# Optimization experiments

Measured on AMD Instinct MI355X. Metric: run time of the kernel, lower is better.

Reference implementation:

```python
import jax, jax.numpy as jnp
import numpy as np

B, T, N, C = 64, 256, 21, 3
HID, HEADS, HDIM, DOUT = 128, 4, 32, 256
CDIM, DMODEL = 64, 256
DINNER, DSTATE, DCONV, DTRANK, L = 512, 16, 4, 16, 4
NSIGNS, NHS, NLOC, NMOV, NORI = 2000, 40, 20, 20, 8
TEMP = 0.07

def _ln(x, w):
    mu = x.mean(-1, keepdims=True)
    var = ((x - mu) ** 2).mean(-1, keepdims=True)
    return (x - mu) / jnp.sqrt(var + 1e-5) * w

def _silu(x):
    return x * jax.nn.sigmoid(x)

def _causal_conv(u, w, b):  # u:(B,T,D), depthwise causal conv, w:(D,K)
    K = w.shape[1]
    up = jnp.pad(u, ((0, 0), (K - 1, 0), (0, 0)))
    y = sum(up[:, k:k + u.shape[1], :] * w[:, k] for k in range(K))
    return y + b

def _scan(u, dt, Bm, Cm, A, Dp):  # selective SSM scan; u,dt:(B,T,Di), Bm,Cm:(B,T,Ds)
    def step(h, xs):
        dt_t, b_t, c_t, u_t = xs
        dA = jnp.exp(dt_t[..., None] * A)                       # (B,Di,Ds)
        dBu = dt_t[..., None] * b_t[:, None, :] * u_t[..., None]
        h = dA * h + dBu
        y = jnp.einsum('bds,bs->bd', h, c_t)
        return h, y
    h0 = jnp.zeros((u.shape[0], A.shape[0], A.shape[1]), u.dtype)
    xs = (dt.swapaxes(0, 1), Bm.swapaxes(0, 1), Cm.swapaxes(0, 1), u.swapaxes(0, 1))
    _, ys = jax.lax.scan(step, h0, xs)
    return ys.swapaxes(0, 1) + u * Dp

def _cos_logits(f, p):
    fn = f / (jnp.linalg.norm(f, axis=-1, keepdims=True) + 1e-8)
    pn = p / (jnp.linalg.norm(p, axis=-1, keepdims=True) + 1e-8)
    return fn @ pn.T / TEMP

def _forward(x, agan_w_in, agan_b_in, agan_w_gat, agan_a_src, agan_a_dst,
             agan_w_out, agan_b_out, pdm_w, pdm_b, pdm_w_fuse, pdm_b_fuse,
             ssm_ln_w, ssm_in_proj, ssm_conv_w, ssm_conv_b, ssm_x_proj,
             ssm_dt_w, ssm_dt_b, ssm_A_log, ssm_D, ssm_out_proj,
             hpc_w_sign, hpc_b_sign, sign_protos, proto_hs, proto_loc,
             proto_mov, proto_ori):
    # ---- AGAN: multi-head graph attention over N landmarks per frame ----
    h0 = jax.nn.relu(x @ agan_w_in + agan_b_in)                  # (B,T,N,HID)
    h = jnp.einsum('btni,hio->btnho', h0, agan_w_gat)            # (B,T,N,H,O)
    src = jnp.einsum('btnho,ho->btnh', h, agan_a_src)
    dst = jnp.einsum('btnho,ho->btnh', h, agan_a_dst)
    e = jax.nn.leaky_relu(src[:, :, :, None, :] + dst[:, :, None, :, :], 0.2)  # (B,T,Ni,Nj,H)
    alpha = jax.nn.softmax(e, axis=3)
    agg = jnp.einsum('btijh,btjho->btiho', alpha, h).reshape(h0.shape)
    feat = jax.nn.relu(h0 + agg)
    spatial = (feat @ agan_w_out + agan_b_out).mean(axis=2)      # (B,T,DOUT)
    # ---- PDM: 4 phonological component projections + fusion ----
    comps = jax.nn.relu(jnp.einsum('btd,kdc->btkc', spatial, pdm_w) + pdm_b)  # (B,T,4,CDIM)
    fused = comps.reshape(B, T, 4 * CDIM) @ pdm_w_fuse + pdm_b_fuse           # (B,T,DMODEL)
    # ---- BiSSM: bidirectional selective SSM layers with residuals ----
    xx = fused
    for l in range(L):
        xn = _ln(xx, ssm_ln_w[l])
        ysum = 0.0
        for d in range(2):
            u_in = xn if d == 0 else xn[:, ::-1]
            xz = u_in @ ssm_in_proj[l, d]
            u, z = xz[..., :DINNER], xz[..., DINNER:]
            u = _silu(_causal_conv(u, ssm_conv_w[l, d], ssm_conv_b[l, d]))
            xdbl = u @ ssm_x_proj[l, d]
            dt = jax.nn.softplus(xdbl[..., :DTRANK] @ ssm_dt_w[l, d] + ssm_dt_b[l, d])
            Bm = xdbl[..., DTRANK:DTRANK + DSTATE]
            Cm = xdbl[..., DTRANK + DSTATE:]
            A = -jnp.exp(ssm_A_log[l, d])
            y = _scan(u, dt, Bm, Cm, A, ssm_D[l, d]) * _silu(z)
            y = y @ ssm_out_proj[l, d]
            ysum = ysum + (y if d == 0 else y[:, ::-1])
        xx = xx + ysum
    temporal = xx
    # ---- HPC: prototype classifier ----
    emb = temporal.mean(axis=1) @ hpc_w_sign + hpc_b_sign        # (B,DMODEL)
    logits = _cos_logits(emb, sign_protos)                       # (B,NSIGNS)
    pooled_c = comps.mean(axis=1)                                # (B,4,CDIM)
    sims = tuple(_cos_logits(pooled_c[:, k], p)
                 for k, p in enumerate((proto_hs, proto_loc, proto_mov, proto_ori)))
    return (logits, emb) + sims

def setup_inputs():
    key = jax.random.key(0)
    ks = iter(jax.random.split(key, 40))
    def rn(shape, scale):
        return jax.random.normal(next(ks), shape, jnp.float32) * scale
    inp = {}
    inp['x'] = rn((B, T, N, C), 1.0)
    inp['agan_w_in'] = rn((C, HID), C ** -0.5)
    inp['agan_b_in'] = jnp.zeros((HID,), jnp.float32)
    inp['agan_w_gat'] = rn((HEADS, HID, HDIM), HID ** -0.5)
    inp['agan_a_src'] = rn((HEADS, HDIM), 0.1)
    inp['agan_a_dst'] = rn((HEADS, HDIM), 0.1)
    inp['agan_w_out'] = rn((HID, DOUT), HID ** -0.5)
    inp['agan_b_out'] = jnp.zeros((DOUT,), jnp.float32)
    inp['pdm_w'] = rn((4, DOUT, CDIM), DOUT ** -0.5)
    inp['pdm_b'] = jnp.zeros((4, CDIM), jnp.float32)
    inp['pdm_w_fuse'] = rn((4 * CDIM, DMODEL), (4 * CDIM) ** -0.5)
    inp['pdm_b_fuse'] = jnp.zeros((DMODEL,), jnp.float32)
    inp['ssm_ln_w'] = jnp.ones((L, DMODEL), jnp.float32)
    inp['ssm_in_proj'] = rn((L, 2, DMODEL, 2 * DINNER), DMODEL ** -0.5)
    inp['ssm_conv_w'] = rn((L, 2, DINNER, DCONV), DCONV ** -0.5)
    inp['ssm_conv_b'] = jnp.zeros((L, 2, DINNER), jnp.float32)
    inp['ssm_x_proj'] = rn((L, 2, DINNER, DTRANK + 2 * DSTATE), DINNER ** -0.5)
    inp['ssm_dt_w'] = rn((L, 2, DTRANK, DINNER), DTRANK ** -0.5)
    inp['ssm_dt_b'] = jnp.full((L, 2, DINNER), -4.6, jnp.float32)  # softplus ~ 0.01
    a = jnp.log(jnp.tile(jnp.arange(1, DSTATE + 1, dtype=jnp.float32)[None, :], (DINNER, 1)))
    inp['ssm_A_log'] = jnp.tile(a[None, None], (L, 2, 1, 1))
    inp['ssm_D'] = jnp.ones((L, 2, DINNER), jnp.float32)
    inp['ssm_out_proj'] = rn((L, 2, DINNER, DMODEL), DINNER ** -0.5)
    inp['hpc_w_sign'] = rn((DMODEL, DMODEL), DMODEL ** -0.5)
    inp['hpc_b_sign'] = jnp.zeros((DMODEL,), jnp.float32)
    inp['sign_protos'] = rn((NSIGNS, DMODEL), 1.0)
    inp['proto_hs'] = rn((NHS, CDIM), 1.0)
    inp['proto_loc'] = rn((NLOC, CDIM), 1.0)
    inp['proto_mov'] = rn((NMOV, CDIM), 1.0)
    inp['proto_ori'] = rn((NORI, CDIM), 1.0)
    return inp

def reference(x, agan_w_in, agan_b_in, agan_w_gat, agan_a_src, agan_a_dst,
              agan_w_out, agan_b_out, pdm_w, pdm_b, pdm_w_fuse, pdm_b_fuse,
              ssm_ln_w, ssm_in_proj, ssm_conv_w, ssm_conv_b, ssm_x_proj,
              ssm_dt_w, ssm_dt_b, ssm_A_log, ssm_D, ssm_out_proj,
              hpc_w_sign, hpc_b_sign, sign_protos, proto_hs, proto_loc,
              proto_mov, proto_ori):
    return _forward(x, agan_w_in, agan_b_in, agan_w_gat, agan_a_src, agan_a_dst,
                    agan_w_out, agan_b_out, pdm_w, pdm_b, pdm_w_fuse, pdm_b_fuse,
                    ssm_ln_w, ssm_in_proj, ssm_conv_w, ssm_conv_b, ssm_x_proj,
                    ssm_dt_w, ssm_dt_b, ssm_A_log, ssm_D, ssm_out_proj,
                    hpc_w_sign, hpc_b_sign, sign_protos, proto_hs, proto_loc,
                    proto_mov, proto_ori)
```

## Files before the change

kernel.cpp:

```cpp
#include <hip/hip_runtime.h>
#include <hip/hip_bf16.h>
#include <math.h>

#define BB 64
#define TT 256
#define NNODE 21
#define HID 128
#define DMODEL 256
#define DINNER 512
#define NSIGNS 2000
#define BTT (BB*TT)

typedef unsigned short u16;
typedef unsigned int u32;
typedef __attribute__((ext_vector_type(8))) short short8;
typedef __attribute__((ext_vector_type(4))) float f32x4;

template<int V> struct IC { static constexpr int v = V; };

__device__ __forceinline__ float siluf(float x){ return x/(1.f+expf(-x)); }
__device__ __forceinline__ u16 f2bf(float x){ __hip_bfloat16 h = __float2bfloat16(x); return *(u16*)&h; }
__device__ __forceinline__ u32 pk2bf(float a, float b){
  float2 f2; f2.x = a; f2.y = b;
  __hip_bfloat162 h2 = __float22bfloat162_rn(f2);
  return *(u32*)&h2;
}
__device__ __forceinline__ float bf2f(u16 u){ return __uint_as_float(((u32)u)<<16); }
__device__ __forceinline__ void gload16(const u16* g, u16* l){
  __builtin_amdgcn_global_load_lds((const __attribute__((address_space(1))) void*)g,
                                   (__attribute__((address_space(3))) void*)l, 16, 0, 0);
}

__global__ __launch_bounds__(256) void transpose_w_kernel(
    const float* __restrict__ in_proj, const float* __restrict__ out_proj,
    const float* __restrict__ x_proj, const float* __restrict__ w_out,
    const float* __restrict__ pdm_w, const float* __restrict__ w_fuse,
    const float* __restrict__ w_gat, const float* __restrict__ a_src,
    const float* __restrict__ a_dst, u16* __restrict__ dst)
{
  __shared__ short tl[64*66];
  int bx = blockIdx.x, tid = threadIdx.x;
  if (bx == 944) {
    for (int j = tid; j < 2048; j += 256) {
      int c = j >> 7, i = j & 127;
      float v = 0.f;
      if (c < 8) {
        int which = c >> 2, h = c & 3;
        const float* a = (which ? a_dst : a_src) + h*32;
        const float* wg = w_gat + (size_t)h*4096 + i*32;
        #pragma unroll
        for (int o=0;o<32;++o) v += wg[o]*a[o];
      }
      dst[3850240 + j] = f2bf(v);
    }
    return;
  }
  const float* S = nullptr; size_t soff = 0; int lds = 0, Nsrc = 0;
  size_t doff = 0; int ldd = 0, Nout = 0;
  int tn = 0, tk = 0;
  if (bx < 512) {
    int j = bx >> 5, tt = bx & 31;
    int l = j >> 2, d = j & 1, zh = (j >> 1) & 1;
    tn = tt >> 2; tk = tt & 3;
    S = in_proj; soff = ((size_t)(l*2+d)*256)*1024 + zh*512; lds = 1024; Nsrc = 512;
    doff = (size_t)l*524288 + (size_t)(zh*1024 + d*512)*256; ldd = 256; Nout = 512;
  } else if (bx < 768) {
    int j = (bx-512) >> 5, tt = (bx-512) & 31;
    int l = j >> 1, d = j & 1;
    tn = tt >> 3; tk = tt & 7;
    S = out_proj; soff = (size_t)(l*2+d)*512*256; lds = 256; Nsrc = 256;
    doff = 2097152 + (size_t)l*262144 + d*512; ldd = 1024; Nout = 256;
  } else if (bx < 896) {
    int r = bx - 768;
    if (r >= 64) return;
    int j = r >> 3;
    int l = j >> 1, d = j & 1;
    tn = 0; tk = r & 7;
    S = x_proj; soff = (size_t)(l*2+d)*512*48; lds = 48; Nsrc = 48;
    doff = 3145728 + (size_t)l*131072 + (size_t)d*32768; ldd = 512; Nout = 64;
  } else if (bx < 904) {
    int tt = bx-896; tn = tt>>1; tk = tt&1;
    S = w_out; soff = 0; lds = 256; Nsrc = 256;
    doff = 3670016; ldd = 128; Nout = 256;
  } else if (bx < 920) {
    int j = (bx-904)>>2, tt = (bx-904)&3;
    tn = 0; tk = tt;
    S = pdm_w; soff = (size_t)j*16384; lds = 64; Nsrc = 64;
    doff = 3702784 + (size_t)j*16384; ldd = 256; Nout = 64;
  } else if (bx < 936) {
    int tt = bx-920; tn = tt>>2; tk = tt&3;
    S = w_fuse; soff = 0; lds = 256; Nsrc = 256;
    doff = 3768320; ldd = 256; Nout = 256;
  } else {
    int j = (bx-936)>>1, tt = (bx-936)&1;
    tn = 0; tk = tt;
    S = w_gat; soff = (size_t)j*4096; lds = 32; Nsrc = 32;
    doff = 3833856 + (size_t)j*4096; ldd = 128; Nout = 32;
  }
  int n0 = tn*64, k0 = tk*64;
  #pragma unroll
  for (int i=0;i<16;++i){
    int kk = i*4 + (tid>>6), nn = tid&63;
    float v = (n0+nn < Nsrc) ? S[soff + (size_t)(k0+kk)*lds + n0+nn] : 0.f;
    tl[nn*66+kk] = (short)f2bf(v);
  }
  __syncthreads();
  #pragma unroll
  for (int i=0;i<16;++i){
    int nn = i*4 + (tid>>6), kk = tid&63;
    if (n0+nn < Nout) dst[doff + (size_t)(n0+nn)*ldd + k0+kk] = (u16)tl[nn*66+kk];
  }
}

__global__ __launch_bounds__(256) void agan_kernel(
    const float* __restrict__ x, const float* __restrict__ w_in, const float* __restrict__ b_in,
    const u16* __restrict__ bpt, const u16* __restrict__ wsd,
    u16* __restrict__ fsum_out)
{
  int bt = blockIdx.x;
  int tid = threadIdx.x;
  int lane = tid & 63, wid = tid >> 6;
  int lr = lane & 15, lq = lane >> 4;
  __shared__ float xv[NNODE][4];
  __shared__ __align__(16) short sh0[32*136];
  __shared__ __align__(16) short hmT[128*40];
  __shared__ __align__(16) short alb[4*32*40];
  __shared__ float sd[2][NNODE][4];
  __shared__ float sm[4][NNODE];
  short8 bp[4][2];
  #pragma unroll
  for (int ks=0;ks<4;++ks)
    #pragma unroll
    for (int ct=0;ct<2;++ct)
      bp[ks][ct] = *(const short8*)(bpt + (size_t)(wid*32+ct*16+lr)*128 + ks*32 + lq*8);
  int ii = tid & 127, nn0 = tid >> 7;
  float w0 = w_in[ii], w1 = w_in[128+ii], w2 = w_in[256+ii], bi = b_in[ii];
  if (tid < NNODE*3) xv[tid/3][tid%3] = x[(size_t)bt*63 + tid];
  __syncthreads();
  #pragma unroll
  for (int n = 0; n < 32; n += 2) {
    int nr = n + nn0;
    float v = 0.f;
    if (nr < NNODE)
      v = fmaxf(bi + xv[nr][0]*w0 + xv[nr][1]*w1 + xv[nr][2]*w2, 0.f);
    sh0[nr*136 + ii] = (short)f2bf(v);
  }
  __syncthreads();
  {
    f32x4 g00={},g01={},g10={},g11={},s0v={},s1v={};
    #pragma unroll
    for (int ks=0;ks<4;++ks){
      short8 a0 = *(const short8*)&sh0[(lr   )*136 + ks*32 + lq*8];
      short8 a1 = *(const short8*)&sh0[(16+lr)*136 + ks*32 + lq*8];
      g00 = __builtin_amdgcn_mfma_f32_16x16x32_bf16(a0, bp[ks][0], g00, 0,0,0);
      g01 = __builtin_amdgcn_mfma_f32_16x16x32_bf16(a0, bp[ks][1], g01, 0,0,0);
      g10 = __builtin_amdgcn_mfma_f32_16x16x32_bf16(a1, bp[ks][0], g10, 0,0,0);
      g11 = __builtin_amdgcn_mfma_f32_16x16x32_bf16(a1, bp[ks][1], g11, 0,0,0);
      if (wid == 0) {
        short8 wb = *(const short8*)(wsd + (size_t)lr*128 + ks*32 + lq*8);
        s0v = __builtin_amdgcn_mfma_f32_16x16x32_bf16(a0, wb, s0v, 0,0,0);
        s1v = __builtin_amdgcn_mfma_f32_16x16x32_bf16(a1, wb, s1v, 0,0,0);
      }
    }
    f32x4 gg[2][2] = {{g00,g01},{g10,g11}};
    #pragma unroll
    for (int mt=0;mt<2;++mt)
      #pragma unroll
      for (int ct=0;ct<2;++ct){
        int col = wid*32 + ct*16 + lr;
        int row0 = mt*16 + lq*4;
        u32 wv0 = pk2bf(gg[mt][ct][0], gg[mt][ct][1]);
        u32 wv1 = pk2bf(gg[mt][ct][2], gg[mt][ct][3]);
        *(uint2*)&hmT[col*40 + row0] = make_uint2(wv0,wv1);
      }
    if (wid == 0 && lr < 8) {
      int which = lr >> 2, h = lr & 3;
      #pragma unroll
      for (int r=0;r<4;++r){
        int n0_ = lq*4 + r, n1_ = 16 + lq*4 + r;
        if (n0_ < NNODE) sd[which][n0_][h] = s0v[r];
        if (n1_ < NNODE) sd[which][n1_][h] = s1v[r];
      }
    }
  }
  __syncthreads();
  for (int idx = tid; idx < 84*32; idx += 256) {
    int j = idx & 31, ih = idx >> 5;
    int i = ih >> 2, h = ih & 3;
    float e = -1e30f;
    if (j < NNODE){
      e = sd[0][i][h] + sd[1][j][h];
      e = e>=0.f ? e : 0.2f*e;
    }
    float m = e;
    #pragma unroll
    for (int off=1; off<32; off<<=1) m = fmaxf(m, __shfl_xor(m, off));
    float ex = (j < NNODE) ? __expf(e - m) : 0.f;
    alb[(h*32+i)*40 + j] = (short)f2bf(ex);
    float s = ex;
    #pragma unroll
    for (int off=1; off<32; off<<=1) s += __shfl_xor(s, off);
    if (j == 0) sm[h][i] = 1.f/s;
  }
  __syncthreads();
  {
    int h = wid;
    short8 a0 = *(const short8*)&alb[(h*32 + lr     )*40 + lq*8];
    short8 a1 = *(const short8*)&alb[(h*32 + 16 + lr)*40 + lq*8];
    short8 b0 = *(const short8*)&hmT[(h*32 + lr     )*40 + lq*8];
    short8 b1 = *(const short8*)&hmT[(h*32 + 16 + lr)*40 + lq*8];
    f32x4 c00={},c01={},c10={},c11={};
    c00 = __builtin_amdgcn_mfma_f32_16x16x32_bf16(a0,b0,c00,0,0,0);
    c01 = __builtin_amdgcn_mfma_f32_16x16x32_bf16(a0,b1,c01,0,0,0);
    c10 = __builtin_amdgcn_mfma_f32_16x16x32_bf16(a1,b0,c10,0,0,0);
    c11 = __builtin_amdgcn_mfma_f32_16x16x32_bf16(a1,b1,c11,0,0,0);
    f32x4 cc[2][2] = {{c00,c01},{c10,c11}};
    #pragma unroll
    for (int ct=0; ct<2; ++ct){
      int col = h*32 + ct*16 + lr;
      float s = 0.f;
      #pragma unroll
      for (int mt=0; mt<2; ++mt)
        #pragma unroll
        for (int r=0;r<4;++r){
          int n = mt*16 + lq*4 + r;
          if (n < NNODE)
            s += fmaxf(bf2f((u16)sh0[n*136+col]) + cc[mt][ct][r]*sm[h][n], 0.f);
        }
      s += __shfl_xor(s, 16);
      s += __shfl_xor(s, 32);
      if (lq == 0) fsum_out[(size_t)bt*128 + col] = f2bf(s*(1.f/21.f));
    }
  }
}

template<int ACC, int BIAS, int RELU, int SM>
__global__ __launch_bounds__(256) void gemm_bf16_kernel(
    const u16* __restrict__ A, const u16* __restrict__ BT, const float* __restrict__ bias,
    float* __restrict__ C, u16* __restrict__ C2,
    int M, int N, int K, int lda)
{
  __shared__ __align__(16) short Asl[8192];
  __shared__ __align__(16) short Bsl[8192];
  int tid = threadIdx.x;
  int lane = tid & 63, wid = tid >> 6;
  int wm = wid >> 1, wn = wid & 1;
  int row0 = blockIdx.y*128, col0 = blockIdx.x*128;
  const u16* Ab = A  + (size_t)row0*lda;
  const u16* Bb = BT + (size_t)col0*K;
  f32x4 acc[4][4] = {};
  int lrow = lane & 15, lk = (lane>>4)*8;
  for (int k0 = 0; k0 < K; k0 += 64) {
    #pragma unroll
    for (int is=0; is<4; ++is){
      int li = is*256 + tid;
      int row = li >> 3;
      int c8  = (li & 7) ^ (row & 7);
      gload16(Ab + (size_t)row*lda + k0 + c8*8, (u16*)Asl + ((is<<8)+(wid<<6))*8);
      gload16(Bb + (size_t)row*K   + k0 + c8*8, (u16*)Bsl + ((is<<8)+(wid<<6))*8);
    }
    __syncthreads();
    #pragma unroll
    for (int ksub=0; ksub<2; ++ksub){
      int slot = (ksub*32 + lk) >> 3;
      short8 a[4], b[4];
      #pragma unroll
      for (int i=0;i<4;++i){ int rr=wm*64+i*16+lrow; a[i]=*(const short8*)&Asl[rr*64+((slot^(rr&7))<<3)]; }
      #pragma unroll
      for (int j=0;j<4;++j){ int rr=wn*64+j*16+lrow; b[j]=*(const short8*)&Bsl[rr*64+((slot^(rr&7))<<3)]; }
      #pragma unroll
      for (int i=0;i<4;++i)
        #pragma unroll
        for (int j=0;j<4;++j)
          acc[i][j] = __builtin_amdgcn_mfma_f32_16x16x32_bf16(a[i], b[j], acc[i][j], 0, 0, 0);
    }
    __syncthreads();
  }
  #pragma unroll
  for (int i=0;i<4;++i) {
    int row = row0 + wm*64 + i*16 + (lane>>4)*4;
    #pragma unroll
    for (int j=0;j<4;++j) {
      int col = col0 + wn*64 + j*16 + (lane&15);
      if (col < N) {
        float bv = BIAS ? bias[col] : 0.f;
        #pragma unroll
        for (int r=0;r<4;++r) {
          float v = acc[i][j][r] + bv;
          if (RELU) v = fmaxf(v, 0.f);
          size_t o = (size_t)(row+r)*N + col;
          if (ACC)           C[o] += v;
          else if (SM == 0)  C[o]  = v;
          else               C2[o] = f2bf(v);
        }
      }
    }
  }
}

template<int ACC, int BIAS, int RELU, int SM, int POOL>
__global__ __launch_bounds__(256) void gemm_bm64_kernel(
    const u16* __restrict__ A, const u16* __restrict__ BT, const float* __restrict__ bias,
    float* __restrict__ C, u16* __restrict__ C2, float* __restrict__ pool,
    int M, int N, int K, int lda)
{
  __shared__ __align__(16) short Asl[4096];
  __shared__ __align__(16) short Bsl[8192];
  int tid = threadIdx.x;
  int lane = tid & 63, wid = tid >> 6;
  int wm = wid >> 1, wn = wid & 1;
  int row0 = blockIdx.y*64, col0 = blockIdx.x*128;
  const u16* Ab = A  + (size_t)row0*lda;
  const u16* Bb = BT + (size_t)col0*K;
  f32x4 acc[2][4] = {};
  int lrow = lane & 15, lq = lane >> 4, lk = lq*8;
  for (int k0 = 0; k0 < K; k0 += 64) {
    #pragma unroll
    for (int is=0; is<2; ++is){
      int li = is*256 + tid;
      int row = li >> 3;
      int c8  = (li & 7) ^ (row & 7);
      gload16(Ab + (size_t)row*lda + k0 + c8*8, (u16*)Asl + ((is<<8)+(wid<<6))*8);
    }
    #pragma unroll
    for (int is=0; is<4; ++is){
      int li = is*256 + tid;
      int row = li >> 3;
      int c8  = (li & 7) ^ (row & 7);
      gload16(Bb + (size_t)row*K + k0 + c8*8, (u16*)Bsl + ((is<<8)+(wid<<6))*8);
    }
    __syncthreads();
    #pragma unroll
    for (int ksub=0; ksub<2; ++ksub){
      int slot = (ksub*32 + lk) >> 3;
      short8 a[2], b[4];
      #pragma unroll
      for (int i=0;i<2;++i){ int rr=wm*32+i*16+lrow; a[i]=*(const short8*)&Asl[rr*64+((slot^(rr&7))<<3)]; }
      #pragma unroll
      for (int j=0;j<4;++j){ int rr=wn*64+j*16+lrow; b[j]=*(const short8*)&Bsl[rr*64+((slot^(rr&7))<<3)]; }
      #pragma unroll
      for (int i=0;i<2;++i)
        #pragma unroll
        for (int j=0;j<4;++j)
          acc[i][j] = __builtin_amdgcn_mfma_f32_16x16x32_bf16(a[i], b[j], acc[i][j], 0, 0, 0);
    }
    __syncthreads();
  }
  float colsum[4] = {0.f,0.f,0.f,0.f};
  #pragma unroll
  for (int i=0;i<2;++i) {
    int row = row0 + wm*32 + i*16 + lq*4;
    #pragma unroll
    for (int j=0;j<4;++j) {
      int col = col0 + wn*64 + j*16 + lrow;
      if (col < N) {
        float bv = BIAS ? bias[col] : 0.f;
        #pragma unroll
        for (int r=0;r<4;++r) {
          float v = acc[i][j][r] + bv;
          if (RELU) v = fmaxf(v, 0.f);
          size_t o = (size_t)(row+r)*N + col;
          if (ACC)           C[o] += v;
          else if (SM == 0)  C[o]  = v;
          else               C2[o] = f2bf(v);
          if (POOL) colsum[j] += v;
        }
      }
    }
  }
  if (POOL) {
    float* red = (float*)Asl;
    #pragma unroll
    for (int j=0;j<4;++j) red[tid*4+j] = colsum[j];
    __syncthreads();
    if (tid < 128) {
      int wn_ = tid >> 6, j_ = (tid >> 4) & 3, l15 = tid & 15;
      float s = 0.f;
      #pragma unroll
      for (int wm_=0;wm_<2;++wm_)
        #pragma unroll
        for (int g=0;g<4;++g)
          s += red[(((wm_*2+wn_)*64) + g*16 + l15)*4 + j_];
      pool[(size_t)blockIdx.y*256 + blockIdx.x*128 + tid] = s * (1.f/256.f);
    }
  }
}

__global__ __launch_bounds__(256) void gemm_xproj_kernel(
    const u16* __restrict__ A, const u16* __restrict__ BT, float* __restrict__ C)
{
  __shared__ __align__(16) short Asl[4096];
  __shared__ __align__(16) short Bsl[4096];
  int tid = threadIdx.x;
  int lane = tid & 63, wid = tid >> 6;
  int lrow = lane & 15, lq = lane >> 4, lk = lq*8;
  int d = blockIdx.x, row0 = blockIdx.y*64;
  const u16* Ab = A  + (size_t)row0*1024 + d*512;
  const u16* Bb = BT + (size_t)d*32768;
  f32x4 acc[4] = {};
  for (int k0 = 0; k0 < 512; k0 += 64) {
    #pragma unroll
    for (int is=0; is<2; ++is){
      int li = is*256 + tid;
      int row = li >> 3;
      int c8  = (li & 7) ^ (row & 7);
      gload16(Ab + (size_t)row*1024 + k0 + c8*8, (u16*)Asl + ((is<<8)+(wid<<6))*8);
      gload16(Bb + (size_t)row*512  + k0 + c8*8, (u16*)Bsl + ((is<<8)+(wid<<6))*8);
    }
    __syncthreads();
    #pragma unroll
    for (int ksub=0; ksub<2; ++ksub){
      int slot = (ksub*32 + lk) >> 3;
      int arr = wid*16 + lrow;
      short8 av = *(const short8*)&Asl[arr*64 + ((slot^(arr&7))<<3)];
      #pragma unroll
      for (int j=0;j<4;++j){
        int brr = j*16 + lrow;
        short8 bv = *(const short8*)&Bsl[brr*64 + ((slot^(brr&7))<<3)];
        acc[j] = __builtin_amdgcn_mfma_f32_16x16x32_bf16(av, bv, acc[j], 0, 0, 0);
      }
    }
    __syncthreads();
  }
  #pragma unroll
  for (int j=0;j<4;++j){
    int col = d*64 + j*16 + lrow;
    #pragma unroll
    for (int r=0;r<4;++r){
      int row = row0 + wid*16 + lq*4 + r;
      C[(size_t)row*128 + col] = acc[j][r];
    }
  }
}

__global__ __launch_bounds__(256) void ln_kernel(const float* __restrict__ x,
    const float* __restrict__ w, u16* __restrict__ o)
{
  int row = blockIdx.x*4 + (threadIdx.x>>6);
  int lane = threadIdx.x & 63;
  float4 v = *(const float4*)(x + (size_t)row*DMODEL + lane*4);
  float s = v.x+v.y+v.z+v.w;
  #pragma unroll
  for (int off=32;off>=1;off>>=1) s += __shfl_xor(s, off);
  float mu = s * (1.f/256.f);
  float d0=v.x-mu, d1=v.y-mu, d2=v.z-mu, d3=v.w-mu;
  float q = d0*d0+d1*d1+d2*d2+d3*d3;
  #pragma unroll
  for (int off=32;off>=1;off>>=1) q += __shfl_xor(q, off);
  float inv = 1.f/sqrtf(q*(1.f/256.f) + 1e-5f);
  float4 wv = *(const float4*)(w + lane*4);
  uint2 pk; pk.x = pk2bf(d0*inv*wv.x, d1*inv*wv.y); pk.y = pk2bf(d2*inv*wv.z, d3*inv*wv.w);
  *(uint2*)(o + (size_t)row*DMODEL + lane*4) = pk;
}

__global__ __launch_bounds__(256) void conv_kernel(const u16* __restrict__ xz,
    const float* __restrict__ cw, const float* __restrict__ cb,
    u16* __restrict__ ucv)
{
  int idx = blockIdx.x*256 + threadIdx.x;
  int du8 = idx & 127, dir = du8 >> 6, d8 = (du8 & 63) << 3;
  int bt = idx >> 7, t = bt & 255;
  const u16* up = xz + (size_t)(bt - t)*2048 + dir*512 + d8;
  float w[8][4];
  #pragma unroll
  for (int j=0;j<8;++j){
    float4 wv = *(const float4*)(cw + (size_t)dir*2048 + (d8+j)*4);
    w[j][0]=wv.x; w[j][1]=wv.y; w[j][2]=wv.z; w[j][3]=wv.w;
  }
  float s[8];
  float4 cb0 = *(const float4*)(cb + dir*512 + d8);
  float4 cb1 = *(const float4*)(cb + dir*512 + d8 + 4);
  s[0]=cb0.x; s[1]=cb0.y; s[2]=cb0.z; s[3]=cb0.w;
  s[4]=cb1.x; s[5]=cb1.y; s[6]=cb1.z; s[7]=cb1.w;
  if (dir == 0) {
    #pragma unroll
    for (int k=0;k<4;++k){
      int tk = t-3+k;
      if (tk >= 0){
        short8 uv = *(const short8*)(up + (size_t)tk*2048);
        #pragma unroll
        for (int j=0;j<8;++j) s[j] += w[j][k]*bf2f((u16)uv[j]);
      }
    }
  } else {
    #pragma unroll
    for (int kk=0;kk<4;++kk){
      int tk = t+kk;
      if (tk < TT){
        short8 uv = *(const short8*)(up + (size_t)tk*2048);
        #pragma unroll
        for (int j=0;j<8;++j) s[j] += w[j][3-kk]*bf2f((u16)uv[j]);
      }
    }
  }
  short8 o;
  #pragma unroll
  for (int j=0;j<8;++j) o[j] = (short)f2bf(siluf(s[j]));
  *(short8*)(ucv + (size_t)bt*1024 + dir*512 + d8) = o;
}

template<int FINAL>
__global__ __launch_bounds__(256) void scan_phase_kernel(
    const u16* __restrict__ ucv, const float* __restrict__ xd, const u16* __restrict__ xz,
    const float* __restrict__ dtw, const float* __restrict__ dtb,
    const float* __restrict__ alog, const float* __restrict__ dvec,
    const u16* __restrict__ hend_r, const float* __restrict__ sdt_r,
    float* __restrict__ sdt_w, u16* __restrict__ hend_w,
    u16* __restrict__ yout)
{
  int b = blockIdx.x, c = blockIdx.y, gz = blockIdx.z;
  int d = gz >> 1;
  int tid = threadIdx.x;
  int dd = ((gz & 1) << 8) + tid;
  float wdt[16], Av[16], h[16];
  #pragma unroll
  for (int s=0;s<16;++s){
    wdt[s] = dtw[d*8192 + s*512 + dd];
    Av[s]  = -__expf(alog[d*8192 + dd*16 + s]);
    h[s]   = 0.f;
  }
  float bdt = dtb[d*512 + dd];
  bool powok = true;
  #pragma unroll
  for (int s=0;s<16;++s) powok = powok && (fabsf(Av[s] + (float)(s+1)) < 1e-5f*(float)(s+1));
  __shared__ float sxd[32][48];
  if (FINAL) {
    for (int i = tid; i < 1536; i += 256){
      int q = i/48, r = i - q*48;
      int p = (c<<5)+q, t = d ? 255-p : p;
      sxd[q][r] = xd[((size_t)b*TT + t)*128 + d*64 + r];
    }
  } else {
    for (int i = tid; i < 1024; i += 256){
      int q = i>>5, r = i&31;
      int p = (c<<5)+q, t = d ? 255-p : p;
      sxd[q][r] = xd[((size_t)b*TT + t)*128 + d*64 + r];
    }
  }
  if (FINAL) {
    if (powok) {
      for (int cp=0; cp<c; ++cp){
        size_t cbase = (((size_t)b*8+cp)*2+d)*512 + dd;
        float S = sdt_r[cbase];
        float e1 = __expf(-S);
        short8 h0v = *(const short8*)(hend_r + cbase*16);
        short8 h1v = *(const short8*)(hend_r + cbase*16 + 8);
        float pw = e1;
        #pragma unroll
        for (int s=0;s<8;++s){ h[s] = fmaf(pw, h[s], bf2f((u16)h0v[s])); pw *= e1; }
        #pragma unroll
        for (int s=0;s<8;++s){ h[s+8] = fmaf(pw, h[s+8], bf2f((u16)h1v[s])); pw *= e1; }
      }
    } else {
      for (int cp=0; cp<c; ++cp){
        size_t cbase = (((size_t)b*8+cp)*2+d)*512 + dd;
        float S = sdt_r[cbase];
        short8 h0v = *(const short8*)(hend_r + cbase*16);
        short8 h1v = *(const short8*)(hend_r + cbase*16 + 8);
        #pragma unroll
        for (int s=0;s<8;++s)  h[s]   = fmaf(__expf(Av[s]*S),   h[s],   bf2f((u16)h0v[s]));
        #pragma unroll
        for (int s=0;s<8;++s)  h[s+8] = fmaf(__expf(Av[s+8]*S), h[s+8], bf2f((u16)h1v[s]));
      }
    }
  }
  __syncthreads();
  float S = 0.f;
  float Dv = FINAL ? dvec[d*512 + dd] : 0.f;
  const u16* ub = ucv + d*512 + dd;
  const u16* zb = xz + 1024 + d*512 + dd;
  u16* yb = yout + d*512 + dd;
  auto qloop = [&](auto icpow){
    constexpr int POW = decltype(icpow)::v;
    #pragma unroll 4
    for (int q=0;q<32;++q) {
      int p = (c<<5)+q, t = d ? 255-p : p;
      size_t row = (size_t)b*TT + t;
      float uc = bf2f(ub[row*1024]);
      float zc = FINAL ? bf2f(zb[row*2048]) : 0.f;
      const float* sr = sxd[q];
      float p0=0.f,p1=0.f,p2=0.f,p3=0.f;
      #pragma unroll
      for (int r=0;r<16;r+=4){
        p0 = fmaf(sr[r+0],wdt[r+0],p0);
        p1 = fmaf(sr[r+1],wdt[r+1],p1);
        p2 = fmaf(sr[r+2],wdt[r+2],p2);
        p3 = fmaf(sr[r+3],wdt[r+3],p3);
      }
      float dtp = bdt + ((p0+p1)+(p2+p3));
      float dt = fmaxf(dtp,0.f) + __logf(1.f + __expf(-fabsf(dtp)));
      float dtu = dt*uc;
      if (!FINAL) S += dt;
      float y0=0.f, y1=0.f;
      if (POW) {
        float rr = __expf(-dt);
        float pw = rr;
        #pragma unroll
        for (int s=0;s<16;++s){
          h[s] = fmaf(pw, h[s], dtu*sr[16+s]);
          if (FINAL) y0 = fmaf(h[s], sr[32+s], y0);
          pw *= rr;
        }
      } else {
        #pragma unroll
        for (int s=0;s<16;s+=2){
          float dA0 = __expf(dt*Av[s]);
          float dA1 = __expf(dt*Av[s+1]);
          h[s]   = fmaf(dA0, h[s],   dtu*sr[16+s]);
          h[s+1] = fmaf(dA1, h[s+1], dtu*sr[16+s+1]);
          if (FINAL){ y0 = fmaf(h[s],sr[32+s],y0); y1 = fmaf(h[s+1],sr[32+s+1],y1); }
        }
      }
      if (FINAL){
        float yv = (y0+y1) + uc*Dv;
        float sg = zc / (1.f + __expf(-zc));
        yb[row*2048] = f2bf(yv*sg);
      }
    }
  };
  if (powok) qloop(IC<1>{}); else qloop(IC<0>{});
  if (!FINAL){
    size_t co = (((size_t)b*8+c)*2+d)*512 + dd;
    sdt_w[co] = S;
    short8 o0, o1;
    #pragma unroll
    for (int s=0;s<8;++s){ o0[s] = (short)f2bf(h[s]); o1[s] = (short)f2bf(h[s+8]); }
    *(short8*)(hend_w + co*16)     = o0;
    *(short8*)(hend_w + co*16 + 8) = o1;
  }
}

__global__ __launch_bounds__(256) void emb_kernel(const float* __restrict__ xx,
    const float* __restrict__ wsgn, const float* __restrict__ bsgn,
    float* __restrict__ embw, float* __restrict__ out)
{
  int b = blockIdx.x, tid = threadIdx.x;
  __shared__ float mt[256];
  float s0=0.f,s1=0.f,s2=0.f,s3=0.f;
  for (int t=0;t<TT;t+=4){
    s0 += xx[((size_t)b*TT+t  )*DMODEL + tid];
    s1 += xx[((size_t)b*TT+t+1)*DMODEL + tid];
    s2 += xx[((size_t)b*TT+t+2)*DMODEL + tid];
    s3 += xx[((size_t)b*TT+t+3)*DMODEL + tid];
  }
  mt[tid] = (s0+s1+s2+s3)*(1.f/256.f);
  __syncthreads();
  float acc = bsgn[tid];
  for (int i=0;i<DMODEL;++i) acc += mt[i]*wsgn[i*DMODEL + tid];
  embw[b*DMODEL+tid] = acc;
  out[128000 + b*DMODEL + tid] = acc;
}

__global__ __launch_bounds__(256) void head_kernel(const float* __restrict__ embw,
    const float* __restrict__ protos, const float* __restrict__ part,
    const float* __restrict__ phs, const float* __restrict__ ploc,
    const float* __restrict__ pmov, const float* __restrict__ pori,
    float* __restrict__ out)
{
  int b = blockIdx.x, qt = blockIdx.y, tid = threadIdx.x;
  __shared__ __align__(16) float e[256];
  __shared__ float red[4];
  if (qt == 4) {
    e[tid] = part[(size_t)(4*b)*256 + tid] + part[(size_t)(4*b+1)*256 + tid]
           + part[(size_t)(4*b+2)*256 + tid] + part[(size_t)(4*b+3)*256 + tid];
    __syncthreads();
    if (tid < 4) {
      float ss = 0.f;
      for (int i=0;i<64;++i){ float q = e[tid*64+i]; ss += q*q; }
      red[tid] = 1.f/(sqrtf(ss)+1e-8f);
    }
    __syncthreads();
    if (tid < 88) {
      int k, pi; const float* P; size_t off; int npk;
      if (tid < 40)      { k=0; pi=tid;    P=phs;  off=144384; npk=40; }
      else if (tid < 60) { k=1; pi=tid-40; P=ploc; off=146944; npk=20; }
      else if (tid < 80) { k=2; pi=tid-60; P=pmov; off=148224; npk=20; }
      else               { k=3; pi=tid-80; P=pori; off=149504; npk=8;  }
      float dot=0.f, ps=0.f;
      for (int i=0;i<64;++i){ float pv = P[pi*64+i]; dot += pv*e[k*64+i]; ps += pv*pv; }
      out[off + (size_t)b*npk + pi] = dot*red[k]/(sqrtf(ps)+1e-8f)*(1.f/0.07f);
    }
    return;
  }
  float acc = embw[b*DMODEL + tid];
  e[tid] = acc;
  __syncthreads();
  float v = acc*acc;
  #pragma unroll
  for (int off=32;off>=1;off>>=1) v += __shfl_xor(v, off);
  if ((tid&63)==0) red[tid>>6] = v;
  __syncthreads();
  float esc = 1.f/(sqrtf(red[0]+red[1]+red[2]+red[3]) + 1e-8f);
  int pend = qt*500 + 500;
  for (int p = qt*500 + tid; p < pend; p += 256) {
    const float* pr = protos + (size_t)p*256;
    float dot=0.f, ps=0.f;
    for (int i=0;i<256;i+=4) {
      float4 pv = *(const float4*)(pr+i);
      float4 ev = *(const float4*)(e+i);
      dot += pv.x*ev.x + pv.y*ev.y + pv.z*ev.z + pv.w*ev.w;
      ps  += pv.x*pv.x + pv.y*pv.y + pv.z*pv.z + pv.w*pv.w;
    }
    out[(size_t)b*NSIGNS + p] = dot*esc/(sqrtf(ps)+1e-8f)*(1.f/0.07f);
  }
}

extern "C" void kernel_launch(void* const* d_in, const int* in_sizes, int n_in,
                              void* d_out, int out_size, void* d_ws, size_t ws_size,
                              hipStream_t stream) {
  const float* x         = (const float*)d_in[0];
  const float* w_in      = (const float*)d_in[1];
  const float* b_in      = (const float*)d_in[2];
  const float* w_gat     = (const float*)d_in[3];
  const float* a_src     = (const float*)d_in[4];
  const float* a_dst     = (const float*)d_in[5];
  const float* w_out     = (const float*)d_in[6];
  const float* b_out     = (const float*)d_in[7];
  const float* pdm_w     = (const float*)d_in[8];
  const float* pdm_b     = (const float*)d_in[9];
  const float* w_fuse    = (const float*)d_in[10];
  const float* b_fuse    = (const float*)d_in[11];
  const float* ln_w      = (const float*)d_in[12];
  const float* in_proj   = (const float*)d_in[13];
  const float* conv_w    = (const float*)d_in[14];
  const float* conv_b    = (const float*)d_in[15];
  const float* x_proj    = (const float*)d_in[16];
  const float* dt_w      = (const float*)d_in[17];
  const float* dt_b      = (const float*)d_in[18];
  const float* A_log     = (const float*)d_in[19];
  const float* Dvec      = (const float*)d_in[20];
  const float* out_proj  = (const float*)d_in[21];
  const float* w_sign    = (const float*)d_in[22];
  const float* b_sign    = (const float*)d_in[23];
  const float* protos    = (const float*)d_in[24];
  const float* phs       = (const float*)d_in[25];
  const float* ploc      = (const float*)d_in[26];
  const float* pmov      = (const float*)d_in[27];
  const float* pori      = (const float*)d_in[28];
  float* out = (float*)d_out;

  float* wsf = (float*)d_ws;
  const size_t f_xx    = 0;
  const size_t f_xdbl  = f_xx   + 4194304;
  const size_t f_part  = f_xdbl + 2097152;
  const size_t f_emb   = f_part + 65536;
  const size_t f_end   = f_emb  + 16384;
  u16* wsu = (u16*)(wsf + f_end);
  const size_t u_xn    = 0;
  const size_t u_xz    = u_xn   + 4194304;
  const size_t u_ucv   = u_xz   + 33554432;
  const size_t u_fsum  = u_ucv  + 16777216;
  const size_t u_spat  = u_fsum + 2097152;
  const size_t u_comps = u_spat + 4194304;
  const size_t u_w     = u_comps+ 4194304;
  u16* wiT = wsu + u_w;
  u16* woT = wiT + 2097152;
  u16* wxT = woT + 1048576;
  u16* wA  = wxT + 524288;
  u16* wB  = wA  + 32768;
  u16* wF  = wB  + 65536;
  u16* wBp = wF  + 65536;
  u16* wSd = wBp + 16384;
  u16*   hstate = wsu + u_fsum;
  float* sdt    = (float*)(wsu + u_fsum + 8388608);

  transpose_w_kernel<<<945, 256, 0, stream>>>(in_proj, out_proj, x_proj, w_out, pdm_w, w_fuse, w_gat, a_src, a_dst, wsu + u_w);
  agan_kernel<<<BTT, 256, 0, stream>>>(x, w_in, b_in, wBp, wSd, wsu + u_fsum);
  gemm_bm64_kernel<0,1,0,1,0><<<dim3(2,256), 256, 0, stream>>>(wsu+u_fsum, wA, b_out, nullptr, wsu+u_spat, nullptr, BTT, 256, 128, 128);
  gemm_bm64_kernel<0,1,1,1,1><<<dim3(2,256), 256, 0, stream>>>(wsu+u_spat, wB, pdm_b, nullptr, wsu+u_comps, wsf+f_part, BTT, 256, 256, 256);
  gemm_bm64_kernel<0,1,0,0,0><<<dim3(2,256), 256, 0, stream>>>(wsu+u_comps, wF, b_fuse, wsf+f_xx, nullptr, nullptr, BTT, 256, 256, 256);

  for (int l = 0; l < 4; ++l) {
    ln_kernel<<<BTT/4, 256, 0, stream>>>(wsf+f_xx, ln_w + l*DMODEL, wsu+u_xn);
    gemm_bf16_kernel<0,0,0,1><<<dim3(16,128), 256, 0, stream>>>(wsu+u_xn, wiT + (size_t)l*524288,
        nullptr, nullptr, wsu+u_xz, BTT, 2048, 256, 256);
    conv_kernel<<<BTT*128/256, 256, 0, stream>>>(wsu+u_xz, conv_w + (size_t)l*4096,
        conv_b + (size_t)l*1024, wsu+u_ucv);
    gemm_xproj_kernel<<<dim3(2,256), 256, 0, stream>>>(wsu+u_ucv, wxT + (size_t)l*131072, wsf+f_xdbl);
    scan_phase_kernel<0><<<dim3(64,7,4), 256, 0, stream>>>(wsu+u_ucv, wsf+f_xdbl, nullptr,
        dt_w + (size_t)l*16384, dt_b + (size_t)l*1024,
        A_log + (size_t)l*16384, nullptr,
        nullptr, nullptr, sdt, hstate, nullptr);
    scan_phase_kernel<1><<<dim3(64,8,4), 256, 0, stream>>>(wsu+u_ucv, wsf+f_xdbl, wsu+u_xz,
        dt_w + (size_t)l*16384, dt_b + (size_t)l*1024,
        A_log + (size_t)l*16384, Dvec + (size_t)l*1024,
        hstate, sdt, nullptr, nullptr, wsu+u_xz);
    gemm_bm64_kernel<1,0,0,0,0><<<dim3(2,256), 256, 0, stream>>>(wsu+u_xz, woT + (size_t)l*262144,
        nullptr, wsf+f_xx, nullptr, nullptr, BTT, 256, 1024, 2048);
  }

  emb_kernel<<<64, 256, 0, stream>>>(wsf+f_xx, w_sign, b_sign, wsf+f_emb, out);
  head_kernel<<<dim3(64,5), 256, 0, stream>>>(wsf+f_emb, protos, wsf+f_part, phs, ploc, pmov, pori, out);
  (void)in_sizes; (void)n_in; (void)out_size; (void)ws_size;
}
```

Baseline: 1.144 ms.

## Replace two-phase chunked SSM scan with single-pass double-buffered scan

```diff
diff --git a/kernel.cpp b/kernel.cpp
--- a/kernel.cpp
+++ b/kernel.cpp
@@ -184,18 +184,28 @@
     }
   }
   __syncthreads();
+  if (tid < 84) {
+    int i = tid >> 2, h = tid & 3;
+    float sv = sd[0][i][h], m = -1e30f;
+    #pragma unroll
+    for (int j=0;j<NNODE;++j){
+      float e = sv + sd[1][j][h];
+      e = e>=0.f ? e : 0.2f*e;
+      m = fmaxf(m,e);
+    }
+    sm[h][i] = m;
+  }
+  __syncthreads();
   for (int idx = tid; idx < 84*32; idx += 256) {
     int j = idx & 31, ih = idx >> 5;
     int i = ih >> 2, h = ih & 3;
-    float e = -1e30f;
+    float m = sm[h][i];
+    float ex = 0.f;
     if (j < NNODE){
-      e = sd[0][i][h] + sd[1][j][h];
+      float e = sd[0][i][h] + sd[1][j][h];
       e = e>=0.f ? e : 0.2f*e;
-    }
-    float m = e;
-    #pragma unroll
-    for (int off=1; off<32; off<<=1) m = fmaxf(m, __shfl_xor(m, off));
-    float ex = (j < NNODE) ? __expf(e - m) : 0.f;
+      ex = __expf(e - m);
+    }
     alb[(h*32+i)*40 + j] = (short)f2bf(ex);
     float s = ex;
     #pragma unroll
@@ -499,16 +509,13 @@
   *(short8*)(ucv + (size_t)bt*1024 + dir*512 + d8) = o;
 }
 
-template<int FINAL>
-__global__ __launch_bounds__(256) void scan_phase_kernel(
+__global__ __launch_bounds__(256) void scan_full_kernel(
     const u16* __restrict__ ucv, const float* __restrict__ xd, const u16* __restrict__ xz,
     const float* __restrict__ dtw, const float* __restrict__ dtb,
     const float* __restrict__ alog, const float* __restrict__ dvec,
-    const u16* __restrict__ hend_r, const float* __restrict__ sdt_r,
-    float* __restrict__ sdt_w, u16* __restrict__ hend_w,
     u16* __restrict__ yout)
 {
-  int b = blockIdx.x, c = blockIdx.y, gz = blockIdx.z;
+  int b = blockIdx.x, gz = blockIdx.y;
   int d = gz >> 1;
   int tid = threadIdx.x;
   int dd = ((gz & 1) << 8) + tid;
@@ -520,113 +527,82 @@
     h[s]   = 0.f;
   }
   float bdt = dtb[d*512 + dd];
+  float Dv  = dvec[d*512 + dd];
   bool powok = true;
   #pragma unroll
   for (int s=0;s<16;++s) powok = powok && (fabsf(Av[s] + (float)(s+1)) < 1e-5f*(float)(s+1));
-  __shared__ float sxd[32][48];
-  if (FINAL) {
-    for (int i = tid; i < 1536; i += 256){
-      int q = i/48, r = i - q*48;
-      int p = (c<<5)+q, t = d ? 255-p : p;
-      sxd[q][r] = xd[((size_t)b*TT + t)*128 + d*64 + r];
-    }
-  } else {
-    for (int i = tid; i < 1024; i += 256){
-      int q = i>>5, r = i&31;
-      int p = (c<<5)+q, t = d ? 255-p : p;
-      sxd[q][r] = xd[((size_t)b*TT + t)*128 + d*64 + r];
-    }
-  }
-  if (FINAL) {
-    if (powok) {
-      for (int cp=0; cp<c; ++cp){
-        size_t cbase = (((size_t)b*8+cp)*2+d)*512 + dd;
-        float S = sdt_r[cbase];
-        float e1 = __expf(-S);
-        short8 h0v = *(const short8*)(hend_r + cbase*16);
-        short8 h1v = *(const short8*)(hend_r + cbase*16 + 8);
-        float pw = e1;
-        #pragma unroll
-        for (int s=0;s<8;++s){ h[s] = fmaf(pw, h[s], bf2f((u16)h0v[s])); pw *= e1; }
-        #pragma unroll
-        for (int s=0;s<8;++s){ h[s+8] = fmaf(pw, h[s+8], bf2f((u16)h1v[s])); pw *= e1; }
-      }
-    } else {
-      for (int cp=0; cp<c; ++cp){
-        size_t cbase = (((size_t)b*8+cp)*2+d)*512 + dd;
-        float S = sdt_r[cbase];
-        short8 h0v = *(const short8*)(hend_r + cbase*16);
-        short8 h1v = *(const short8*)(hend_r + cbase*16 + 8);
-        #pragma unroll
-        for (int s=0;s<8;++s)  h[s]   = fmaf(__expf(Av[s]*S),   h[s],   bf2f((u16)h0v[s]));
-        #pragma unroll
-        for (int s=0;s<8;++s)  h[s+8] = fmaf(__expf(Av[s+8]*S), h[s+8], bf2f((u16)h1v[s]));
-      }
-    }
-  }
-  __syncthreads();
-  float S = 0.f;
-  float Dv = FINAL ? dvec[d*512 + dd] : 0.f;
+  __shared__ float sxd[2][16][48];
+  __shared__ u16 su[2][16][256];
+  __shared__ u16 sz[2][16][256];
   const u16* ub = ucv + d*512 + dd;
   const u16* zb = xz + 1024 + d*512 + dd;
   u16* yb = yout + d*512 + dd;
-  auto qloop = [&](auto icpow){
-    constexpr int POW = decltype(icpow)::v;
-    #pragma unroll 4
-    for (int q=0;q<32;++q) {
-      int p = (c<<5)+q, t = d ? 255-p : p;
+  auto STAGE = [&](int nb, int w){
+    #pragma unroll
+    for (int q=0;q<16;++q){
+      int p = (w<<4)+q, t = d ? 255-p : p;
       size_t row = (size_t)b*TT + t;
-      float uc = bf2f(ub[row*1024]);
-      float zc = FINAL ? bf2f(zb[row*2048]) : 0.f;
-      const float* sr = sxd[q];
-      float p0=0.f,p1=0.f,p2=0.f,p3=0.f;
-      #pragma unroll
-      for (int r=0;r<16;r+=4){
-        p0 = fmaf(sr[r+0],wdt[r+0],p0);
-        p1 = fmaf(sr[r+1],wdt[r+1],p1);
-        p2 = fmaf(sr[r+2],wdt[r+2],p2);
-        p3 = fmaf(sr[r+3],wdt[r+3],p3);
-      }
-      float dtp = bdt + ((p0+p1)+(p2+p3));
-      float dt = fmaxf(dtp,0.f) + __logf(1.f + __expf(-fabsf(dtp)));
-      float dtu = dt*uc;
-      if (!FINAL) S += dt;
-      float y0=0.f, y1=0.f;
-      if (POW) {
-        float rr = __expf(-dt);
-        float pw = rr;
-        #pragma unroll
-        for (int s=0;s<16;++s){
-          h[s] = fmaf(pw, h[s], dtu*sr[16+s]);
-          if (FINAL) y0 = fmaf(h[s], sr[32+s], y0);
-          pw *= rr;
+      su[nb][q][tid] = ub[row*1024];
+      sz[nb][q][tid] = zb[row*2048];
+    }
+    for (int i = tid; i < 768; i += 256){
+      int q = i/48, r = i - q*48;
+      int p = (w<<4)+q, t = d ? 255-p : p;
+      sxd[nb][q][r] = xd[((size_t)b*TT + t)*128 + d*64 + r];
+    }
+  };
+  STAGE(0, 0);
+  int buf = 0;
+  for (int w = 0; w < 16; ++w){
+    __syncthreads();
+    if (w < 15) STAGE(buf^1, w+1);
+    auto qloop = [&](auto icpow){
+      constexpr int POW = decltype(icpow)::v;
+      #pragma unroll 2
+      for (int q=0;q<16;++q){
+        int p = (w<<4)+q, t = d ? 255-p : p;
+        size_t row = (size_t)b*TT + t;
+        const float* sr = sxd[buf][q];
+        float uc = bf2f(su[buf][q][tid]);
+        float zc = bf2f(sz[buf][q][tid]);
+        float p0=0.f,p1=0.f,p2=0.f,p3=0.f;
+        #pragma unroll
+        for (int r=0;r<16;r+=4){
+          p0 = fmaf(sr[r+0],wdt[r+0],p0);
+          p1 = fmaf(sr[r+1],wdt[r+1],p1);
+          p2 = fmaf(sr[r+2],wdt[r+2],p2);
+          p3 = fmaf(sr[r+3],wdt[r+3],p3);
         }
-      } else {
-        #pragma unroll
-        for (int s=0;s<16;s+=2){
-          float dA0 = __expf(dt*Av[s]);
-          float dA1 = __expf(dt*Av[s+1]);
-          h[s]   = fmaf(dA0, h[s],   dtu*sr[16+s]);
-          h[s+1] = fmaf(dA1, h[s+1], dtu*sr[16+s+1]);
-          if (FINAL){ y0 = fmaf(h[s],sr[32+s],y0); y1 = fmaf(h[s+1],sr[32+s+1],y1); }
+        float dtp = bdt + ((p0+p1)+(p2+p3));
+        float dt = fmaxf(dtp,0.f) + __logf(1.f + __expf(-fabsf(dtp)));
+        float dtu = dt*uc;
+        float y0=0.f, y1=0.f;
+        if (POW) {
+          float rr = __expf(-dt);
+          float pw = rr;
+          #pragma unroll
+          for (int s=0;s<16;++s){
+            h[s] = fmaf(pw, h[s], dtu*sr[16+s]);
+            y0 = fmaf(h[s], sr[32+s], y0);
+            pw *= rr;
+          }
+        } else {
+          #pragma unroll
+          for (int s=0;s<16;s+=2){
+            float dA0 = __expf(dt*Av[s]);
+            float dA1 = __expf(dt*Av[s+1]);
+            h[s]   = fmaf(dA0, h[s],   dtu*sr[16+s]);
+            h[s+1] = fmaf(dA1, h[s+1], dtu*sr[16+s+1]);
+            y0 = fmaf(h[s],sr[32+s],y0); y1 = fmaf(h[s+1],sr[32+s+1],y1);
+          }
         }
-      }
-      if (FINAL){
         float yv = (y0+y1) + uc*Dv;
         float sg = zc / (1.f + __expf(-zc));
         yb[row*2048] = f2bf(yv*sg);
       }
-    }
-  };
-  if (powok) qloop(IC<1>{}); else qloop(IC<0>{});
-  if (!FINAL){
-    size_t co = (((size_t)b*8+c)*2+d)*512 + dd;
-    sdt_w[co] = S;
-    short8 o0, o1;
-    #pragma unroll
-    for (int s=0;s<8;++s){ o0[s] = (short)f2bf(h[s]); o1[s] = (short)f2bf(h[s+8]); }
-    *(short8*)(hend_w + co*16)     = o0;
-    *(short8*)(hend_w + co*16 + 8) = o1;
+    };
+    if (powok) qloop(IC<1>{}); else qloop(IC<0>{});
+    buf ^= 1;
   }
 }
 
@@ -761,8 +737,6 @@
   u16* wF  = wB  + 65536;
   u16* wBp = wF  + 65536;
   u16* wSd = wBp + 16384;
-  u16*   hstate = wsu + u_fsum;
-  float* sdt    = (float*)(wsu + u_fsum + 8388608);
 
   transpose_w_kernel<<<945, 256, 0, stream>>>(in_proj, out_proj, x_proj, w_out, pdm_w, w_fuse, w_gat, a_src, a_dst, wsu + u_w);
   agan_kernel<<<BTT, 256, 0, stream>>>(x, w_in, b_in, wBp, wSd, wsu + u_fsum);
@@ -777,14 +751,10 @@
     conv_kernel<<<BTT*128/256, 256, 0, stream>>>(wsu+u_xz, conv_w + (size_t)l*4096,
         conv_b + (size_t)l*1024, wsu+u_ucv);
     gemm_xproj_kernel<<<dim3(2,256), 256, 0, stream>>>(wsu+u_ucv, wxT + (size_t)l*131072, wsf+f_xdbl);
-    scan_phase_kernel<0><<<dim3(64,7,4), 256, 0, stream>>>(wsu+u_ucv, wsf+f_xdbl, nullptr,
-        dt_w + (size_t)l*16384, dt_b + (size_t)l*1024,
-        A_log + (size_t)l*16384, nullptr,
-        nullptr, nullptr, sdt, hstate, nullptr);
-    scan_phase_kernel<1><<<dim3(64,8,4), 256, 0, stream>>>(wsu+u_ucv, wsf+f_xdbl, wsu+u_xz,
+    scan_full_kernel<<<dim3(64,4), 256, 0, stream>>>(wsu+u_ucv, wsf+f_xdbl, wsu+u_xz,
         dt_w + (size_t)l*16384, dt_b + (size_t)l*1024,
         A_log + (size_t)l*16384, Dvec + (size_t)l*1024,
-        hstate, sdt, nullptr, nullptr, wsu+u_xz);
+        wsu+u_xz);
     gemm_bm64_kernel<1,0,0,0,0><<<dim3(2,256), 256, 0, stream>>>(wsu+u_xz, woT + (size_t)l*262144,
         nullptr, wsf+f_xx, nullptr, nullptr, BTT, 256, 1024, 2048);
   }
```

After: 1.238 ms. +8.2%, slower.
